# Optimization experiments

Measured on AMD Instinct MI355X. Metric: run time of the kernel, lower is better.

Reference implementation:

```python
import jax, jax.numpy as jnp
import numpy as np

B, S, D, H = 4, 2048, 1024, 16
HD = D // H  # head_dim = 64


def setup_inputs() -> dict:
    key = jax.random.key(0)
    ks = jax.random.split(key, 10)
    scale = 1.0 / np.sqrt(D)
    x = jax.random.normal(ks[0], (B, S, D), dtype=jnp.float32)
    mask = jax.random.randint(ks[1], (B, S, S), 0, 2, dtype=jnp.int32)
    Wq = jax.random.normal(ks[2], (D, D), dtype=jnp.float32) * scale
    Wk = jax.random.normal(ks[3], (D, D), dtype=jnp.float32) * scale
    Wv = jax.random.normal(ks[4], (D, D), dtype=jnp.float32) * scale
    Wo = jax.random.normal(ks[5], (D, D), dtype=jnp.float32) * scale
    bq = jax.random.normal(ks[6], (D,), dtype=jnp.float32) * 0.01
    bk = jax.random.normal(ks[7], (D,), dtype=jnp.float32) * 0.01
    bv = jax.random.normal(ks[8], (D,), dtype=jnp.float32) * 0.01
    bo = jax.random.normal(ks[9], (D,), dtype=jnp.float32) * 0.01
    return {"x": x, "mask": mask, "Wq": Wq, "bq": bq, "Wk": Wk, "bk": bk,
            "Wv": Wv, "bv": bv, "Wo": Wo, "bo": bo}


def reference(x, mask, Wq, bq, Wk, bk, Wv, bv, Wo, bo):
    # QKV projections (nn.Linear: x @ W^T + b; W stored pre-transposed here as [D,D])
    q = x @ Wq + bq  # [B,S,D]
    k = x @ Wk + bk
    v = x @ Wv + bv
    # split heads -> [B,H,S,HD]
    def heads(t):
        return t.reshape(B, S, H, HD).transpose(0, 2, 1, 3)
    q, k, v = heads(q), heads(k), heads(v)
    scores = jnp.einsum('bhqd,bhkd->bhqk', q, k) / jnp.sqrt(jnp.float32(HD))
    # mask: [B,S,S] -> broadcast over heads; positions where mask==0 get -inf
    scores = jnp.where(mask[:, None, :, :] == 0, -jnp.inf, scores)
    attn = jax.nn.softmax(scores, axis=-1)
    attn = jnp.where(jnp.isnan(attn), 0.0, attn)  # nan_to_num(nan=0.0)
    out = jnp.einsum('bhqk,bhkd->bhqd', attn, v)  # [B,H,S,HD]
    out = out.transpose(0, 2, 1, 3).reshape(B, S, D)
    return out @ Wo + bo
```

## Files before the change

### kernel.cpp

```cpp
#include <hip/hip_runtime.h>
#include <hip/hip_bf16.h>
#include <stdint.h>

#define B_  4
#define S_  2048
#define D_  1024
#define H_  16
#define HD_ 64

typedef __attribute__((ext_vector_type(4))) float f32x4;
typedef __attribute__((ext_vector_type(8))) short bf16x8;

typedef const unsigned int __attribute__((address_space(1)))* gas_ptr;
typedef unsigned int __attribute__((address_space(3)))* las_ptr;

__device__ __forceinline__ void async16(const void* g, void* l) {
  __builtin_amdgcn_global_load_lds((gas_ptr)g, (las_ptr)l, 16, 0, 0);
}

__global__ __launch_bounds__(256) void cvt_x(const float* __restrict__ in,
                                             __hip_bfloat16* __restrict__ out,
                                             int n) {
  const int i = (blockIdx.x * blockDim.x + threadIdx.x) * 4;
  if (i >= n) return;
  const float4 v = *(const float4*)(in + i);
  union { ushort4 u; __hip_bfloat16 h[4]; } o;
  o.h[0] = (__hip_bfloat16)v.x;
  o.h[1] = (__hip_bfloat16)v.y;
  o.h[2] = (__hip_bfloat16)v.z;
  o.h[3] = (__hip_bfloat16)v.w;
  *(ushort4*)(out + i) = o.u;
}

__global__ __launch_bounds__(256) void pack_mask(const int* __restrict__ mk,
                                                 unsigned long long* __restrict__ bits) {
  const long long i = (long long)blockIdx.x * 256 + threadIdx.x;
  const unsigned long long b = __ballot(mk[i] != 0);
  if ((threadIdx.x & 63) == 0) bits[i >> 6] = b;
}

__global__ void transpose_w(const float* __restrict__ Wq,
                            const float* __restrict__ Wk,
                            const float* __restrict__ Wv,
                            const float* __restrict__ Wo,
                            __hip_bfloat16* __restrict__ Wt_qkv,
                            __hip_bfloat16* __restrict__ Wt_o) {
  __shared__ float t[32][33];
  const int z = blockIdx.z;
  const float* W = (z == 0) ? Wq : (z == 1) ? Wk : (z == 2) ? Wv : Wo;
  __hip_bfloat16* Wt = (z < 3) ? (Wt_qkv + (size_t)z * D_ * D_) : Wt_o;
  const int x = blockIdx.x * 32 + threadIdx.x;
  const int y = blockIdx.y * 32 + threadIdx.y;
  t[threadIdx.y][threadIdx.x] = W[(size_t)y * D_ + x];
  __syncthreads();
  const int xo = blockIdx.y * 32 + threadIdx.x;
  const int yo = blockIdx.x * 32 + threadIdx.y;
  Wt[(size_t)yo * D_ + xo] = (__hip_bfloat16)t[threadIdx.x][threadIdx.y];
}

__global__ __launch_bounds__(256) void gemm_qkv(
    const __hip_bfloat16* __restrict__ A,
    const __hip_bfloat16* __restrict__ Bt,
    const float* __restrict__ bq,
    const float* __restrict__ bk,
    const float* __restrict__ bv,
    __hip_bfloat16* __restrict__ QKo,
    __hip_bfloat16* __restrict__ Vt) {
  __shared__ __hip_bfloat16 sA[128 * 32];
  __shared__ __hip_bfloat16 sB[128 * 32];
  const int K = 1024;
  const int tid  = threadIdx.x;
  const int wave = tid >> 6;
  const int lane = tid & 63;
  const int quad = lane >> 4;
  const int l16  = lane & 15;
  const int bm = blockIdx.y * 128;
  const int bn = blockIdx.x * 128;
  const int wm = (wave >> 1) * 64;
  const int wn = (wave & 1) * 64;

  const int r0 = wave * 2, r1 = wave * 2 + 1;
  const int lrow = lane >> 2;
  const int lcol = (lane & 3) * 8;

  const __hip_bfloat16* ga0 = A  + (size_t)(bm + r0 * 16 + lrow) * K + lcol;
  const __hip_bfloat16* ga1 = A  + (size_t)(bm + r1 * 16 + lrow) * K + lcol;
  const __hip_bfloat16* gb0 = Bt + (size_t)(bn + r0 * 16 + lrow) * K + lcol;
  const __hip_bfloat16* gb1 = Bt + (size_t)(bn + r1 * 16 + lrow) * K + lcol;
  char* la0 = (char*)sA + r0 * 1024;
  char* la1 = (char*)sA + r1 * 1024;
  char* lb0 = (char*)sB + r0 * 1024;
  char* lb1 = (char*)sB + r1 * 1024;

  const char* pa = (const char*)sA + (wm + l16) * 64 + quad * 16;
  const char* pb = (const char*)sB + (wn + l16) * 64 + quad * 16;

  f32x4 acc[4][4] = {};

  for (int k0 = 0; k0 < K; k0 += 32) {
    async16(ga0 + k0, la0);
    async16(ga1 + k0, la1);
    async16(gb0 + k0, lb0);
    async16(gb1 + k0, lb1);
    __syncthreads();
    bf16x8 af[4], bf[4];
#pragma unroll
    for (int mt = 0; mt < 4; ++mt) af[mt] = *(const bf16x8*)(pa + mt * 1024);
#pragma unroll
    for (int nt = 0; nt < 4; ++nt) bf[nt] = *(const bf16x8*)(pb + nt * 1024);
#pragma unroll
    for (int mt = 0; mt < 4; ++mt)
#pragma unroll
      for (int nt = 0; nt < 4; ++nt)
        acc[mt][nt] = __builtin_amdgcn_mfma_f32_16x16x32_bf16(af[mt], bf[nt], acc[mt][nt], 0, 0, 0);
    __syncthreads();
  }

#pragma unroll
  for (int mt = 0; mt < 4; ++mt) {
    const int row = bm + wm + mt * 16 + quad * 4;
#pragma unroll
    for (int nt = 0; nt < 4; ++nt) {
      const int col = bn + wn + nt * 16 + l16;
      f32x4 v = acc[mt][nt];
      if (col < 2048) {
        const float bias = (col < 1024) ? bq[col] : bk[col - 1024];
#pragma unroll
        for (int r = 0; r < 4; ++r)
          QKo[(size_t)(row + r) * 2048 + col] = (__hip_bfloat16)(v[r] + bias);
      } else {
        const int cv = col - 2048;
        const float bias = bv[cv];
        const int hh = cv >> 6, d = cv & 63;
        const int bb = row >> 11, s0 = row & 2047;
        union { __hip_bfloat16 h[4]; unsigned long long u; } pk;
#pragma unroll
        for (int r = 0; r < 4; ++r) pk.h[r] = (__hip_bfloat16)(v[r] + bias);
        *(unsigned long long*)(Vt + ((size_t)(bb * 16 + hh) * 64 + d) * 2048 + s0) = pk.u;
      }
    }
  }
}

__global__ __launch_bounds__(256) void gemm_out(
    const __hip_bfloat16* __restrict__ A,
    const __hip_bfloat16* __restrict__ Bt,
    const float* __restrict__ b0,
    float* __restrict__ C,
    int N, int K) {
  __shared__ __hip_bfloat16 sA[128 * 32];
  __shared__ __hip_bfloat16 sB[128 * 32];
  const int tid  = threadIdx.x;
  const int wave = tid >> 6;
  const int lane = tid & 63;
  const int quad = lane >> 4;
  const int l16  = lane & 15;
  const int bm = blockIdx.y * 128;
  const int bn = blockIdx.x * 128;
  const int wm = (wave >> 1) * 64;
  const int wn = (wave & 1) * 64;

  const int r0 = wave * 2, r1 = wave * 2 + 1;
  const int lrow = lane >> 2;
  const int lcol = (lane & 3) * 8;

  const __hip_bfloat16* ga0 = A  + (size_t)(bm + r0 * 16 + lrow) * K + lcol;
  const __hip_bfloat16* ga1 = A  + (size_t)(bm + r1 * 16 + lrow) * K + lcol;
  const __hip_bfloat16* gb0 = Bt + (size_t)(bn + r0 * 16 + lrow) * K + lcol;
  const __hip_bfloat16* gb1 = Bt + (size_t)(bn + r1 * 16 + lrow) * K + lcol;
  char* la0 = (char*)sA + r0 * 1024;
  char* la1 = (char*)sA + r1 * 1024;
  char* lb0 = (char*)sB + r0 * 1024;
  char* lb1 = (char*)sB + r1 * 1024;

  const char* pa = (const char*)sA + (wm + l16) * 64 + quad * 16;
  const char* pb = (const char*)sB + (wn + l16) * 64 + quad * 16;

  f32x4 acc[4][4] = {};

  for (int k0 = 0; k0 < K; k0 += 32) {
    async16(ga0 + k0, la0);
    async16(ga1 + k0, la1);
    async16(gb0 + k0, lb0);
    async16(gb1 + k0, lb1);
    __syncthreads();
    bf16x8 af[4], bf[4];
#pragma unroll
    for (int mt = 0; mt < 4; ++mt) af[mt] = *(const bf16x8*)(pa + mt * 1024);
#pragma unroll
    for (int nt = 0; nt < 4; ++nt) bf[nt] = *(const bf16x8*)(pb + nt * 1024);
#pragma unroll
    for (int mt = 0; mt < 4; ++mt)
#pragma unroll
      for (int nt = 0; nt < 4; ++nt)
        acc[mt][nt] = __builtin_amdgcn_mfma_f32_16x16x32_bf16(af[mt], bf[nt], acc[mt][nt], 0, 0, 0);
    __syncthreads();
  }

#pragma unroll
  for (int mt = 0; mt < 4; ++mt) {
    const int row = bm + wm + mt * 16 + quad * 4;
#pragma unroll
    for (int nt = 0; nt < 4; ++nt) {
      const int col = bn + wn + nt * 16 + l16;
      const float bias = b0[col];
      f32x4 v = acc[mt][nt];
#pragma unroll
      for (int r = 0; r < 4; ++r)
        C[(size_t)(row + r) * N + col] = v[r] + bias;
    }
  }
}

__global__ __launch_bounds__(256, 4) void flash_attn(
    const __hip_bfloat16* __restrict__ QK,
    const __hip_bfloat16* __restrict__ Vt,
    const unsigned long long* __restrict__ mbits,
    __hip_bfloat16* __restrict__ O) {
  __shared__ __hip_bfloat16 sK[2][64 * 64];
  __shared__ __hip_bfloat16 sV[2][64 * 64];
  __shared__ __hip_bfloat16 sP[4][16 * 64];

  const int qt = blockIdx.x, h = blockIdx.y, b = blockIdx.z;
  const int tid = threadIdx.x;
  const int wave = tid >> 6, lane = tid & 63, quad = lane >> 4, l16 = lane & 15;
  const int qbase = qt * 128;
  const size_t brow = (size_t)b * S_;
  const int bh = b * H_ + h;
  const float C = 0.18033688f;
  const float MSH = 11.5415606f;

  bf16x8 qf[2][2];
#pragma unroll
  for (int g = 0; g < 2; ++g) {
    const __hip_bfloat16* qrow =
        QK + (brow + qbase + g * 64 + wave * 16 + l16) * 2048 + h * 64;
#pragma unroll
    for (int c = 0; c < 2; ++c)
      qf[g][c] = *(const bf16x8*)(qrow + c * 32 + quad * 8);
  }

  const int srow = lane >> 3;
  const int schk = (lane & 7) ^ srow;
  const __hip_bfloat16* gK0 =
      QK + (brow + wave * 16 + srow) * 2048 + 1024 + h * 64 + schk * 8;
  const __hip_bfloat16* gK1 = gK0 + (size_t)8 * 2048;
  const __hip_bfloat16* gV0 =
      Vt + ((size_t)bh * 64 + wave * 16 + srow) * 2048 + schk * 8;
  const __hip_bfloat16* gV1 = gV0 + (size_t)8 * 2048;
  char* const lK[2] = {(char*)&sK[0][0] + wave * 2048, (char*)&sK[1][0] + wave * 2048};
  char* const lV[2] = {(char*)&sV[0][0] + wave * 2048, (char*)&sV[1][0] + wave * 2048};

  const unsigned long long* mb0 = mbits + (brow + qbase + wave * 16 + l16) * 32;
  const unsigned long long* mb1 = mb0 + (size_t)64 * 32;

  const int xl = l16 & 7;
  const int koff0 = ((quad ^ xl) * 16);
  const int rowb = l16 * 128;

  float lst[2] = {0.f, 0.f};
  f32x4 oacc[2][4] = {};

  async16(gK0, lK[0]);
  async16(gK1, lK[0] + 1024);
  async16(gV0, lV[0]);
  async16(gV1, lV[0] + 1024);
  __syncthreads();

  const int NT = S_ / 64;
  for (int kt = 0; kt < NT; ++kt) {
    const int cur = kt & 1, nxt = cur ^ 1;

    if (kt + 1 < NT) {
      const size_t ko = (size_t)(kt + 1) * 64 * 2048;
      const size_t vo = (size_t)(kt + 1) * 64;
      async16(gK0 + ko, lK[nxt]);
      async16(gK1 + ko, lK[nxt] + 1024);
      async16(gV0 + vo, lV[nxt]);
      async16(gV1 + vo, lV[nxt] + 1024);
    }
    const unsigned long long mw0 = mb0[kt];
    const unsigned long long mw1 = mb1[kt];

    const char* bK = (const char*)&sK[cur][0] + rowb;
    f32x4 st[2][4];
#pragma unroll
    for (int mt = 0; mt < 4; ++mt) {
      const bf16x8 kf0 = *(const bf16x8*)(bK + mt * 2048 + koff0);
      const bf16x8 kf1 = *(const bf16x8*)(bK + mt * 2048 + (koff0 ^ 64));
      f32x4 a0 = {}, a1 = {};
      a0 = __builtin_amdgcn_mfma_f32_16x16x32_bf16(kf0, qf[0][0], a0, 0, 0, 0);
      a0 = __builtin_amdgcn_mfma_f32_16x16x32_bf16(kf1, qf[0][1], a0, 0, 0, 0);
      a1 = __builtin_amdgcn_mfma_f32_16x16x32_bf16(kf0, qf[1][0], a1, 0, 0, 0);
      a1 = __builtin_amdgcn_mfma_f32_16x16x32_bf16(kf1, qf[1][1], a1, 0, 0, 0);
      st[0][mt] = a0;
      st[1][mt] = a1;
    }

    char* const sPw = (char*)&sP[wave][0];
    bf16x8 pf[2][2];
#pragma unroll
    for (int g = 0; g < 2; ++g) {
      const unsigned long long mw = (g == 0) ? mw0 : mw1;
      const unsigned lo = (unsigned)mw >> (quad * 4);
      const unsigned hi = (unsigned)(mw >> 32) >> (quad * 4);
      float sum = 0.f;
      union { __hip_bfloat16 h[4]; unsigned long long u; } pk[4];
#pragma unroll
      for (int mt = 0; mt < 4; ++mt) {
        const unsigned w32 = (mt < 2) ? lo : hi;
#pragma unroll
        for (int r = 0; r < 4; ++r) {
          float p = __builtin_amdgcn_exp2f(st[g][mt][r] * C - MSH);
          const bool ok = (w32 >> ((mt & 1) * 16 + r)) & 1u;
          p = ok ? p : 0.f;
          sum += p;
          pk[mt].h[r] = (__hip_bfloat16)p;
        }
      }
      lst[g] += sum;
#pragma unroll
      for (int mt = 0; mt < 4; ++mt)
        *(unsigned long long*)(sPw + rowb +
                               (((mt * 2 + (quad >> 1)) ^ xl) * 16) +
                               (quad & 1) * 8) = pk[mt].u;
      pf[g][0] = *(const bf16x8*)(sPw + rowb + koff0);
      pf[g][1] = *(const bf16x8*)(sPw + rowb + (koff0 ^ 64));
    }

    const char* bV = (const char*)&sV[cur][0] + rowb;
#pragma unroll
    for (int ht = 0; ht < 4; ++ht) {
      const bf16x8 vf0 = *(const bf16x8*)(bV + ht * 2048 + koff0);
      const bf16x8 vf1 = *(const bf16x8*)(bV + ht * 2048 + (koff0 ^ 64));
      oacc[0][ht] = __builtin_amdgcn_mfma_f32_16x16x32_bf16(vf0, pf[0][0], oacc[0][ht], 0, 0, 0);
      oacc[0][ht] = __builtin_amdgcn_mfma_f32_16x16x32_bf16(vf1, pf[0][1], oacc[0][ht], 0, 0, 0);
      oacc[1][ht] = __builtin_amdgcn_mfma_f32_16x16x32_bf16(vf0, pf[1][0], oacc[1][ht], 0, 0, 0);
      oacc[1][ht] = __builtin_amdgcn_mfma_f32_16x16x32_bf16(vf1, pf[1][1], oacc[1][ht], 0, 0, 0);
    }

    __syncthreads();
  }

#pragma unroll
  for (int g = 0; g < 2; ++g) {
    float l = lst[g];
    l += __shfl_xor(l, 16);
    l += __shfl_xor(l, 32);
    const float inv = (l > 0.f) ? 1.f / l : 0.f;
    __hip_bfloat16* orow =
        O + (brow + qbase + g * 64 + wave * 16 + l16) * 1024 + h * 64;
#pragma unroll
    for (int ht = 0; ht < 4; ++ht) {
      union { __hip_bfloat16 h[4]; unsigned long long u; } ok_;
#pragma unroll
      for (int r = 0; r < 4; ++r) ok_.h[r] = (__hip_bfloat16)(oacc[g][ht][r] * inv);
      *(unsigned long long*)(orow + ht * 16 + quad * 4) = ok_.u;
    }
  }
}

extern "C" void kernel_launch(void* const* d_in, const int* in_sizes, int n_in,
                              void* d_out, int out_size, void* d_ws, size_t ws_size,
                              hipStream_t stream) {
  const float* x  = (const float*)d_in[0];
  const int*   mk = (const int*)d_in[1];
  const float* Wq = (const float*)d_in[2];
  const float* bq = (const float*)d_in[3];
  const float* Wk = (const float*)d_in[4];
  const float* bk = (const float*)d_in[5];
  const float* Wv = (const float*)d_in[6];
  const float* bv = (const float*)d_in[7];
  const float* Wo = (const float*)d_in[8];
  const float* bo = (const float*)d_in[9];
  float* out = (float*)d_out;

  __hip_bfloat16* X16    = (__hip_bfloat16*)d_ws;
  __hip_bfloat16* Wt_qkv = X16 + (size_t)B_ * S_ * D_;
  __hip_bfloat16* Wt_o   = Wt_qkv + (size_t)3 * D_ * D_;
  __hip_bfloat16* QK     = Wt_o + (size_t)D_ * D_;
  __hip_bfloat16* Vt     = QK + (size_t)B_ * S_ * 2 * D_;
  __hip_bfloat16* Obuf   = Vt + (size_t)B_ * H_ * HD_ * S_;
  unsigned long long* mbits = (unsigned long long*)(Obuf + (size_t)B_ * S_ * D_);

  const int nx = B_ * S_ * D_;
  cvt_x<<<dim3((nx / 4 + 255) / 256), 256, 0, stream>>>(x, X16, nx);
  transpose_w<<<dim3(32, 32, 4), dim3(32, 32), 0, stream>>>(Wq, Wk, Wv, Wo, Wt_qkv, Wt_o);
  pack_mask<<<dim3((int)((size_t)B_ * S_ * S_ / 256)), 256, 0, stream>>>(mk, mbits);
  gemm_qkv<<<dim3(3 * D_ / 128, B_ * S_ / 128), 256, 0, stream>>>(
      X16, Wt_qkv, bq, bk, bv, QK, Vt);
  flash_attn<<<dim3(S_ / 128, H_, B_), 256, 0, stream>>>(QK, Vt, mbits, Obuf);
  gemm_out<<<dim3(D_ / 128, B_ * S_ / 128), 256, 0, stream>>>(
      Obuf, Wt_o, bo, out, D_, D_);
}
```

Before: 395.3 us.

## Fold softmax scale into Q, compute row sums via MFMA, remap grid

Pre-multiplies Q by the softmax scale (1/sqrt(64)·log2e) in the QKV GEMM epilogue, so the attention inner loop only computes exp2 of the raw score. The fixed max-shift subtraction is dropped, and the per-lane row-sum accumulation plus final shuffles are replaced by MFMAs against an all-ones vector. The grid is flattened so that consecutive blocks walk heads and batches before query tiles, which may improve L2 locality. Mask words are now prefetched one tile ahead, and the K/V pointers advance incrementally. Without the constant shift, exp2 can overflow if scores are large, and rounding Q to bf16 after scaling changes numerics slightly.

```diff
diff --git a/kernel.cpp b/kernel.cpp
--- a/kernel.cpp
+++ b/kernel.cpp
@@ -125,9 +125,10 @@
       f32x4 v = acc[mt][nt];
       if (col < 2048) {
         const float bias = (col < 1024) ? bq[col] : bk[col - 1024];
+        const float sc = (col < 1024) ? 0.18033688011f : 1.0f;
 #pragma unroll
         for (int r = 0; r < 4; ++r)
-          QKo[(size_t)(row + r) * 2048 + col] = (__hip_bfloat16)(v[r] + bias);
+          QKo[(size_t)(row + r) * 2048 + col] = (__hip_bfloat16)((v[r] + bias) * sc);
       } else {
         const int cv = col - 2048;
         const float bias = bv[cv];
@@ -221,14 +222,15 @@
   __shared__ __hip_bfloat16 sV[2][64 * 64];
   __shared__ __hip_bfloat16 sP[4][16 * 64];
 
-  const int qt = blockIdx.x, h = blockIdx.y, b = blockIdx.z;
+  const int bx = blockIdx.x;
+  const int qt = bx >> 6;
+  const int b  = (bx >> 4) & 3;
+  const int h  = bx & 15;
   const int tid = threadIdx.x;
   const int wave = tid >> 6, lane = tid & 63, quad = lane >> 4, l16 = lane & 15;
   const int qbase = qt * 128;
   const size_t brow = (size_t)b * S_;
   const int bh = b * H_ + h;
-  const float C = 0.18033688f;
-  const float MSH = 11.5415606f;
 
   bf16x8 qf[2][2];
 #pragma unroll
@@ -240,14 +242,18 @@
       qf[g][c] = *(const bf16x8*)(qrow + c * 32 + quad * 8);
   }
 
+  bf16x8 vone;
+#pragma unroll
+  for (int j = 0; j < 8; ++j) vone[j] = (short)0x3F80;
+
   const int srow = lane >> 3;
   const int schk = (lane & 7) ^ srow;
-  const __hip_bfloat16* gK0 =
+  const __hip_bfloat16* gk0 =
       QK + (brow + wave * 16 + srow) * 2048 + 1024 + h * 64 + schk * 8;
-  const __hip_bfloat16* gK1 = gK0 + (size_t)8 * 2048;
-  const __hip_bfloat16* gV0 =
+  const __hip_bfloat16* gk1 = gk0 + (size_t)8 * 2048;
+  const __hip_bfloat16* gv0 =
       Vt + ((size_t)bh * 64 + wave * 16 + srow) * 2048 + schk * 8;
-  const __hip_bfloat16* gV1 = gV0 + (size_t)8 * 2048;
+  const __hip_bfloat16* gv1 = gv0 + (size_t)8 * 2048;
   char* const lK[2] = {(char*)&sK[0][0] + wave * 2048, (char*)&sK[1][0] + wave * 2048};
   char* const lV[2] = {(char*)&sV[0][0] + wave * 2048, (char*)&sV[1][0] + wave * 2048};
 
@@ -258,13 +264,16 @@
   const int koff0 = ((quad ^ xl) * 16);
   const int rowb = l16 * 128;
 
-  float lst[2] = {0.f, 0.f};
   f32x4 oacc[2][4] = {};
-
-  async16(gK0, lK[0]);
-  async16(gK1, lK[0] + 1024);
-  async16(gV0, lV[0]);
-  async16(gV1, lV[0] + 1024);
+  f32x4 lacc[2] = {};
+
+  async16(gk0, lK[0]);
+  async16(gk1, lK[0] + 1024);
+  async16(gv0, lV[0]);
+  async16(gv1, lV[0] + 1024);
+  unsigned long long pm0 = mb0[0], pm1 = mb1[0];
+  gk0 += (size_t)64 * 2048; gk1 += (size_t)64 * 2048;
+  gv0 += 64; gv1 += 64;
   __syncthreads();
 
   const int NT = S_ / 64;
@@ -272,15 +281,18 @@
     const int cur = kt & 1, nxt = cur ^ 1;
 
     if (kt + 1 < NT) {
-      const size_t ko = (size_t)(kt + 1) * 64 * 2048;
-      const size_t vo = (size_t)(kt + 1) * 64;
-      async16(gK0 + ko, lK[nxt]);
-      async16(gK1 + ko, lK[nxt] + 1024);
-      async16(gV0 + vo, lV[nxt]);
-      async16(gV1 + vo, lV[nxt] + 1024);
-    }
-    const unsigned long long mw0 = mb0[kt];
-    const unsigned long long mw1 = mb1[kt];
+      async16(gk0, lK[nxt]);
+      async16(gk1, lK[nxt] + 1024);
+      async16(gv0, lV[nxt]);
+      async16(gv1, lV[nxt] + 1024);
+      gk0 += (size_t)64 * 2048; gk1 += (size_t)64 * 2048;
+      gv0 += 64; gv1 += 64;
+    }
+    const unsigned long long mw0 = pm0;
+    const unsigned long long mw1 = pm1;
+    const int kn = (kt + 1 < NT) ? kt + 1 : kt;
+    pm0 = mb0[kn];
+    pm1 = mb1[kn];
 
     const char* bK = (const char*)&sK[cur][0] + rowb;
     f32x4 st[2][4];
@@ -304,21 +316,17 @@
       const unsigned long long mw = (g == 0) ? mw0 : mw1;
       const unsigned lo = (unsigned)mw >> (quad * 4);
       const unsigned hi = (unsigned)(mw >> 32) >> (quad * 4);
-      float sum = 0.f;
       union { __hip_bfloat16 h[4]; unsigned long long u; } pk[4];
 #pragma unroll
       for (int mt = 0; mt < 4; ++mt) {
         const unsigned w32 = (mt < 2) ? lo : hi;
 #pragma unroll
         for (int r = 0; r < 4; ++r) {
-          float p = __builtin_amdgcn_exp2f(st[g][mt][r] * C - MSH);
+          float p = __builtin_amdgcn_exp2f(st[g][mt][r]);
           const bool ok = (w32 >> ((mt & 1) * 16 + r)) & 1u;
-          p = ok ? p : 0.f;
-          sum += p;
-          pk[mt].h[r] = (__hip_bfloat16)p;
+          pk[mt].h[r] = (__hip_bfloat16)(ok ? p : 0.f);
         }
       }
-      lst[g] += sum;
 #pragma unroll
       for (int mt = 0; mt < 4; ++mt)
         *(unsigned long long*)(sPw + rowb +
@@ -326,6 +334,8 @@
                                (quad & 1) * 8) = pk[mt].u;
       pf[g][0] = *(const bf16x8*)(sPw + rowb + koff0);
       pf[g][1] = *(const bf16x8*)(sPw + rowb + (koff0 ^ 64));
+      lacc[g] = __builtin_amdgcn_mfma_f32_16x16x32_bf16(vone, pf[g][0], lacc[g], 0, 0, 0);
+      lacc[g] = __builtin_amdgcn_mfma_f32_16x16x32_bf16(vone, pf[g][1], lacc[g], 0, 0, 0);
     }
 
     const char* bV = (const char*)&sV[cur][0] + rowb;
@@ -344,9 +354,7 @@
 
 #pragma unroll
   for (int g = 0; g < 2; ++g) {
-    float l = lst[g];
-    l += __shfl_xor(l, 16);
-    l += __shfl_xor(l, 32);
+    const float l = lacc[g][0];
     const float inv = (l > 0.f) ? 1.f / l : 0.f;
     __hip_bfloat16* orow =
         O + (brow + qbase + g * 64 + wave * 16 + l16) * 1024 + h * 64;
@@ -389,7 +397,7 @@
   pack_mask<<<dim3((int)((size_t)B_ * S_ * S_ / 256)), 256, 0, stream>>>(mk, mbits);
   gemm_qkv<<<dim3(3 * D_ / 128, B_ * S_ / 128), 256, 0, stream>>>(
       X16, Wt_qkv, bq, bk, bv, QK, Vt);
-  flash_attn<<<dim3(S_ / 128, H_, B_), 256, 0, stream>>>(QK, Vt, mbits, Obuf);
+  flash_attn<<<dim3(S_ / 128 * H_ * B_), 256, 0, stream>>>(QK, Vt, mbits, Obuf);
   gemm_out<<<dim3(D_ / 128, B_ * S_ / 128), 256, 0, stream>>>(
       Obuf, Wt_o, bo, out, D_, D_);
 }
```

Result: slower. 403.2 us (+2.0%).
